# Performance work log

Hardware: AMD Instinct MI355X
Metric: run time of the kernel (lower is better)

Reference implementation:

```python
import jax, jax.numpy as jnp
import numpy as np
import math

LMAX = 3
NCHAN = 32
NEDGE = 50000

# ---------- Wigner 3j (real spherical-harmonic basis), replicating e3nn ----------

def _su2_cg(j1, j2, j3):
    f = math.factorial
    def coeff(m1, m2, m3):
        vmin = int(max(-j1 + j2 + m3, -j1 + m1, 0))
        vmax = int(min(j2 + j3 + m1, j3 - j1 + j2, j3 + m3))
        C = ((2 * j3 + 1) * f(j3 + j1 - j2) * f(j3 - j1 + j2) * f(j1 + j2 - j3) / f(j1 + j2 + j3 + 1)) ** 0.5
        C *= (f(j3 + m3) * f(j3 - m3) * f(j1 - m1) * f(j1 + m1) * f(j2 - m2) * f(j2 + m2)) ** 0.5
        S = 0.0
        for v in range(vmin, vmax + 1):
            S += (-1.0) ** (v + j2 + m2) * f(j2 + j3 + m1 - v) * f(j1 - m1 + v) / (
                f(v) * f(j3 - j1 + j2 - v) * f(j3 + m3 - v) * f(v + j1 - j2 - m3))
        return C * S
    out = np.zeros((2 * j1 + 1, 2 * j2 + 1, 2 * j3 + 1))
    for m1 in range(-j1, j1 + 1):
        for m2 in range(-j2, j2 + 1):
            m3 = m1 + m2
            if -j3 <= m3 <= j3:
                out[m1 + j1, m2 + j2, m3 + j3] = coeff(m1, m2, m3)
    return out

def _q_real_to_complex(l):
    q = np.zeros((2 * l + 1, 2 * l + 1), dtype=np.complex128)
    for m in range(-l, 0):
        q[l + m, l + abs(m)] = 1 / 2 ** 0.5
        q[l + m, l - abs(m)] = -1j / 2 ** 0.5
    q[l, l] = 1.0
    for m in range(1, l + 1):
        q[l + m, l + abs(m)] = (-1) ** m / 2 ** 0.5
        q[l + m, l - abs(m)] = 1j * (-1) ** m / 2 ** 0.5
    return (-1j) ** l * q

def _wigner_3j(l1, l2, l3):
    C = _su2_cg(l1, l2, l3).astype(np.complex128)
    Q1, Q2, Q3 = _q_real_to_complex(l1), _q_real_to_complex(l2), _q_real_to_complex(l3)
    C = np.einsum('ij,kl,mn,ikn->jlm', Q1, Q2, np.conj(Q3.T), C)
    C = np.real(C)
    return C / np.linalg.norm(C)

# ---------- Instruction enumeration (matches the torch module's __init__) ----------

def _build_paths():
    ls = list(range(LMAX + 1))  # irreps 0e,1o,2e,3o -> parity (-1)^l
    ins = []
    for l1 in ls:
        for l2 in ls:
            for l3 in range(abs(l1 - l2), min(l1 + l2, LMAX) + 1):
                if (l1 + l2 + l3) % 2 == 0:  # parity selection p1*p2 == p3
                    ins.append((l1, l2, l3))
    # e3nn Irreps.sort: stable sort of output blocks by ir; pos[i] = sorted position
    order_sorted = sorted(range(len(ins)), key=lambda i: ins[i][2])
    pos = [0] * len(ins)
    for new, old in enumerate(order_sorted):
        pos[old] = new
    # replicate `outputs.insert(ins.i_out, output)` over instruction iteration order
    concat = []
    for idx in range(len(ins)):
        concat.insert(min(pos[idx], len(concat)), idx)
    offs = np.cumsum([0] + [2 * l + 1 for l in ls]).tolist()  # block offsets in dim-16 layout
    # path_weight: component normalization, one path per output block -> sqrt(2*l3+1)
    cg = [jnp.asarray((_wigner_3j(l1, l2, l3) * math.sqrt(2 * l3 + 1)).astype(np.float32))
          for (l1, l2, l3) in ins]
    return ins, pos, concat, offs, cg

_INS, _POS, _CONCAT, _OFFS, _CG = _build_paths()  # 23 instructions, out dim 99


def setup_inputs() -> dict:
    key = jax.random.key(0)
    k1, k2, k3 = jax.random.split(key, 3)
    x = jax.random.normal(k1, (NEDGE, NCHAN, 16), dtype=jnp.float32)
    y = jax.random.normal(k2, (NEDGE, 1, 16), dtype=jnp.float32)
    weights = jax.random.normal(k3, (NEDGE, len(_INS) * NCHAN, 1), dtype=jnp.float32)
    return {"x": x, "y": y, "weights": weights}


def reference(x, y, weights):
    # x: [E, C, 16], y: [E, 1, 16], weights: [E, n_ins*C, 1]
    C = x.shape[1]
    y2 = y[:, 0, :]  # [E, 16]
    outs = [None] * len(_INS)
    for idx, (l1, l2, l3) in enumerate(_INS):
        o1, o2 = _OFFS[l1], _OFFS[l2]
        xb = x[:, :, o1:o1 + 2 * l1 + 1]            # [E, C, 2l1+1]
        yb = y2[:, o2:o2 + 2 * l2 + 1]              # [E, 2l2+1]
        w = weights[:, _POS[idx] * C:(_POS[idx] + 1) * C, 0]  # [E, C]
        # dense CG contraction == sparse gather-multiply-index_add over (mu1,mu2,mu3)
        blk = jnp.einsum('eci,ej,ijk->eck', xb, yb, _CG[idx])  # [E, C, 2l3+1]
        outs[idx] = w[:, :, None] * blk
    return jnp.concatenate([outs[i] for i in _CONCAT], axis=-1)  # [E, C, 99]
```

## Files before the change

### kernel.cpp

```cpp
#include <hip/hip_runtime.h>
#include <math.h>

#define NPATH 23
#define NEDGE 50000
#define NCHAN 32
#define NWROW 736
#define OUTW  99
#define CGTOT 1875
#define TTOT  439
#define EPB   2

constexpr int L1[NPATH]    = {0,0,0,0,1,1,1,1,1,1,2,2,2,2,2,2,2,3,3,3,3,3,3};
constexpr int L2[NPATH]    = {0,1,2,3,0,1,1,2,2,3,0,1,1,2,2,3,3,0,1,2,2,3,3};
constexpr int L3[NPATH]    = {0,1,2,3,1,0,2,1,3,2,2,1,3,0,2,1,3,3,2,1,3,0,2};
constexpr int POS[NPATH]   = {0,4,10,17,5,1,11,6,18,12,13,7,19,2,14,8,20,21,15,9,22,3,16};
constexpr int OOFF[NPATH]  = {0,4,7,12,19,1,34,22,39,46,51,31,61,2,73,25,78,85,68,28,92,3,56};
constexpr int CGOFF[NPATH] = {0,1,10,35,84,93,102,147,192,297,402,427,472,577,602,727,832,1077,1126,1231,1336,1581,1630};
constexpr int TOFF[NPATH]  = {0,1,4,9,16,25,28,43,52,73,88,113,128,163,168,193,208,243,292,327,348,397,404};
constexpr int LOFF[4]      = {0,1,4,9};

constexpr unsigned GMASK[4] = {0xE0010u, 0x700100u, 0x7C00u, 0x182EFu};

__device__ __forceinline__ int imx(int a, int b){ return a > b ? a : b; }
__device__ __forceinline__ int imn(int a, int b){ return a < b ? a : b; }

__device__ __forceinline__ double factd(int n){
    double r = 1.0;
    for(int i = 2; i <= n; ++i) r *= (double)i;
    return r;
}

__global__ __launch_bounds__(512) void cg_setup(float* __restrict__ cg_out){
    const int p  = blockIdx.x;
    const int j1 = L1[p], j2 = L2[p], j3 = L3[p];
    const int n1 = 2*j1+1, n2 = 2*j2+1, n3 = 2*j3+1;
    const int ntot = n1*n2*n3;
    const int t = threadIdx.x;

    __shared__ double scg[343];
    __shared__ double qre[3][49];
    __shared__ double qim[3][49];
    __shared__ double red[512];

    if(t < ntot){
        int a   = t / (n2*n3);
        int rem = t - a*(n2*n3);
        int b   = rem / n3;
        int g   = rem - b*n3;
        int m1 = a - j1, m2 = b - j2, m3 = g - j3;
        double val = 0.0;
        if(m1 + m2 == m3){
            int vmin = imx(imx(-j1 + j2 + m3, -j1 + m1), 0);
            int vmax = imn(imn(j2 + j3 + m1, j3 - j1 + j2), j3 + m3);
            double C = sqrt((2.0*j3 + 1.0) * factd(j3 + j1 - j2) * factd(j3 - j1 + j2)
                            * factd(j1 + j2 - j3) / factd(j1 + j2 + j3 + 1));
            C *= sqrt(factd(j3 + m3) * factd(j3 - m3) * factd(j1 - m1)
                      * factd(j1 + m1) * factd(j2 - m2) * factd(j2 + m2));
            double S = 0.0;
            for(int v = vmin; v <= vmax; ++v){
                double sgn = ((v + j2 + m2) & 1) ? -1.0 : 1.0;
                S += sgn * factd(j2 + j3 + m1 - v) * factd(j1 - m1 + v)
                     / (factd(v) * factd(j3 - j1 + j2 - v) * factd(j3 + m3 - v)
                        * factd(v + j1 - j2 - m3));
            }
            val = C * S;
        }
        scg[t] = val;
    }

    if(t < 3){
        int l = (t == 0) ? j1 : ((t == 1) ? j2 : j3);
        int n = 2*l + 1;
        double* QR = qre[t];
        double* QI = qim[t];
        for(int i = 0; i < 49; ++i){ QR[i] = 0.0; QI[i] = 0.0; }
        const double is2 = 0.70710678118654752440;
        for(int m = -l; m < 0; ++m){
            QR[(l+m)*n + (l-m)] = is2;
            QI[(l+m)*n + (l+m)] = -is2;
        }
        QR[l*n + l] = 1.0;
        for(int m = 1; m <= l; ++m){
            double s = (m & 1) ? -1.0 : 1.0;
            QR[(l+m)*n + (l+m)] = s * is2;
            QI[(l+m)*n + (l-m)] = s * is2;
        }
        double fr, fi;
        switch(l & 3){
            case 0: fr = 1.0;  fi = 0.0;  break;
            case 1: fr = 0.0;  fi = -1.0; break;
            case 2: fr = -1.0; fi = 0.0;  break;
            default: fr = 0.0; fi = 1.0;  break;
        }
        for(int i = 0; i < n*n; ++i){
            double re = QR[i], im = QI[i];
            QR[i] = re*fr - im*fi;
            QI[i] = re*fi + im*fr;
        }
    }
    __syncthreads();

    double val = 0.0;
    if(t < ntot){
        int j   = t / (n2*n3);
        int rem = t - j*(n2*n3);
        int lq  = rem / n3;
        int m   = rem - lq*n3;
        double acc = 0.0;
        for(int i = 0; i < n1; ++i){
            double q1r = qre[0][i*n1 + j], q1i = qim[0][i*n1 + j];
            if(q1r == 0.0 && q1i == 0.0) continue;
            for(int k = 0; k < n2; ++k){
                double q2r = qre[1][k*n2 + lq], q2i = qim[1][k*n2 + lq];
                if(q2r == 0.0 && q2i == 0.0) continue;
                double ar = q1r*q2r - q1i*q2i;
                double ai = q1r*q2i + q1i*q2r;
                for(int n = 0; n < n3; ++n){
                    double cv = scg[(i*n2 + k)*n3 + n];
                    if(cv == 0.0) continue;
                    double q3r = qre[2][n*n3 + m];
                    double q3i = -qim[2][n*n3 + m];
                    acc += cv * (ar*q3r - ai*q3i);
                }
            }
        }
        val = acc;
    }

    red[t] = val * val;
    __syncthreads();
    for(int s = 256; s > 0; s >>= 1){
        if(t < s) red[t] += red[t + s];
        __syncthreads();
    }
    double nrm = sqrt(red[0]);
    if(t < ntot){
        cg_out[CGOFF[p] + t] = (float)(val * sqrt(2.0*j3 + 1.0) / nrm);
    }
}

template<int G>
__device__ __forceinline__ void phaseC(const float* __restrict__ xr,
                                       const float* __restrict__ wreg,
                                       const float* __restrict__ Te,
                                       float* __restrict__ ob)
{
    constexpr unsigned mask = GMASK[G];
    #pragma unroll
    for(int p = 0; p < NPATH; ++p){
        if(!((mask >> p) & 1u)) continue;
        const int n1 = 2*L1[p] + 1;
        const int n3 = 2*L3[p] + 1;
        const int o1 = LOFF[L1[p]];
        const float wp = wreg[p];
        const float* Tp = Te + TOFF[p];
        #pragma unroll
        for(int k = 0; k < n3; ++k){
            float acc = 0.f;
            #pragma unroll
            for(int i = 0; i < n1; ++i)
                acc = fmaf(xr[o1 + i], Tp[i*n3 + k], acc);
            ob[OOFF[p] + k] = wp * acc;
        }
    }
}

__global__ __launch_bounds__(256, 5) void tp_main(
    const float* __restrict__ x, const float* __restrict__ y,
    const float* __restrict__ w, const float* __restrict__ cg,
    float* __restrict__ out)
{
    __shared__ __align__(16) float obuf[EPB*NCHAN*OUTW];
    __shared__ float Ts[EPB*TTOT];
    __shared__ float ys[EPB*16];

    const int tid = threadIdx.x;
    const int e0  = blockIdx.x * EPB;

    const int c   = tid & 31;
    const int el  = (tid >> 5) & 1;
    const int grp = tid >> 6;
    const int e   = e0 + el;

    const float4* xp = reinterpret_cast<const float4*>(x + (size_t)(e*NCHAN + c)*16);
    float4 x0 = xp[0], x1 = xp[1], x2 = xp[2], x3 = xp[3];

    const float* wrow = w + (size_t)e*NWROW + c;
    float wreg[NPATH];
    #pragma unroll
    for(int p = 0; p < NPATH; ++p)
        wreg[p] = wrow[POS[p]*NCHAN];

    if(tid < EPB*16) ys[tid] = y[e0*16 + tid];
    __syncthreads();

    for(int u = tid; u < EPB*TTOT; u += 256){
        int eli = u / TTOT;
        int v   = u - eli*TTOT;
        int p   = 0;
        while(p < NPATH-1 && TOFF[p+1] <= v) ++p;
        int rel = v - TOFF[p];
        int n2  = 2*L2[p] + 1;
        int n3  = 2*L3[p] + 1;
        int i   = rel / n3;
        int k   = rel - i*n3;
        int o2  = LOFF[L2[p]];
        const float* cgp = &cg[CGOFF[p]];
        float acc = 0.f;
        for(int j = 0; j < n2; ++j)
            acc += ys[eli*16 + o2 + j] * cgp[(i*n2 + j)*n3 + k];
        Ts[u] = acc;
    }
    __syncthreads();

    float xr[16];
    xr[0]=x0.x;  xr[1]=x0.y;  xr[2]=x0.z;  xr[3]=x0.w;
    xr[4]=x1.x;  xr[5]=x1.y;  xr[6]=x1.z;  xr[7]=x1.w;
    xr[8]=x2.x;  xr[9]=x2.y;  xr[10]=x2.z; xr[11]=x2.w;
    xr[12]=x3.x; xr[13]=x3.y; xr[14]=x3.z; xr[15]=x3.w;

    const float* Te = Ts + el*TTOT;
    float* ob = obuf + el*(NCHAN*OUTW) + c*OUTW;

    switch(grp){
        case 0: phaseC<0>(xr, wreg, Te, ob); break;
        case 1: phaseC<1>(xr, wreg, Te, ob); break;
        case 2: phaseC<2>(xr, wreg, Te, ob); break;
        default: phaseC<3>(xr, wreg, Te, ob); break;
    }
    __syncthreads();

    const float4* ob4 = reinterpret_cast<const float4*>(obuf);
    float4* o4 = reinterpret_cast<float4*>(out + (size_t)blockIdx.x * (EPB*NCHAN*OUTW));
    #pragma unroll
    for(int idx = tid; idx < EPB*NCHAN*OUTW/4; idx += 256)
        o4[idx] = ob4[idx];
}

extern "C" void kernel_launch(void* const* d_in, const int* in_sizes, int n_in,
                              void* d_out, int out_size, void* d_ws, size_t ws_size,
                              hipStream_t stream)
{
    const float* x  = (const float*)d_in[0];
    const float* y  = (const float*)d_in[1];
    const float* wt = (const float*)d_in[2];
    float* out = (float*)d_out;
    float* cgw = (float*)d_ws;

    cg_setup<<<NPATH, 512, 0, stream>>>(cgw);
    tp_main<<<NEDGE/EPB, 256, 0, stream>>>(x, y, wt, cgw, out);
}
```

Baseline: 285.1 us.

## Stage output tile in fp16, densify CG table, trim per-group weight loads

The shared-memory output staging buffer becomes _Float16 and is widened back to fp32 when written to global memory, halving LDS footprint so more blocks fit per CU (launch bounds raised to 8 blocks). The CG setup now emits a dense 16-wide padded row per (path,i,k) slot, so the per-edge T computation becomes a fixed unrolled 16-term dot with no path search. Each thread group also loads only the weights for its own paths (at most 10) through a precomputed offset table instead of all 23. Rounding outputs through fp16 loses precision and may exceed tolerance.

```diff
diff --git a/kernel.cpp b/kernel.cpp
--- a/kernel.cpp
+++ b/kernel.cpp
@@ -6,20 +6,27 @@
 #define NCHAN 32
 #define NWROW 736
 #define OUTW  99
-#define CGTOT 1875
 #define TTOT  439
 #define EPB   2
+#define NTHR  256
 
 constexpr int L1[NPATH]    = {0,0,0,0,1,1,1,1,1,1,2,2,2,2,2,2,2,3,3,3,3,3,3};
 constexpr int L2[NPATH]    = {0,1,2,3,0,1,1,2,2,3,0,1,1,2,2,3,3,0,1,2,2,3,3};
 constexpr int L3[NPATH]    = {0,1,2,3,1,0,2,1,3,2,2,1,3,0,2,1,3,3,2,1,3,0,2};
 constexpr int POS[NPATH]   = {0,4,10,17,5,1,11,6,18,12,13,7,19,2,14,8,20,21,15,9,22,3,16};
 constexpr int OOFF[NPATH]  = {0,4,7,12,19,1,34,22,39,46,51,31,61,2,73,25,78,85,68,28,92,3,56};
-constexpr int CGOFF[NPATH] = {0,1,10,35,84,93,102,147,192,297,402,427,472,577,602,727,832,1077,1126,1231,1336,1581,1630};
 constexpr int TOFF[NPATH]  = {0,1,4,9,16,25,28,43,52,73,88,113,128,163,168,193,208,243,292,327,348,397,404};
 constexpr int LOFF[4]      = {0,1,4,9};
 
-constexpr unsigned GMASK[4] = {0xE0010u, 0x700100u, 0x7C00u, 0x182EFu};
+constexpr unsigned GMASK4[4] = {0xE0010u, 0x700100u, 0x7C00u, 0x182EFu};
+constexpr int GWOFF[4][10] = {
+    {160, 672, 480, 288,   0,   0,   0,   0,   0,   0},
+    {576, 704,  96, 512,   0,   0,   0,   0,   0,   0},
+    {416, 224, 608,  64, 448,   0,   0,   0,   0,   0},
+    {  0, 128, 320, 544,  32, 352, 192, 384, 256, 640},
+};
+
+typedef _Float16 __attribute__((ext_vector_type(4))) h4;
 
 __device__ __forceinline__ int imx(int a, int b){ return a > b ? a : b; }
 __device__ __forceinline__ int imn(int a, int b){ return a < b ? a : b; }
@@ -30,10 +37,11 @@
     return r;
 }
 
-__global__ __launch_bounds__(512) void cg_setup(float* __restrict__ cg_out){
+__global__ __launch_bounds__(512) void cg_setup(float* __restrict__ cgd2){
     const int p  = blockIdx.x;
     const int j1 = L1[p], j2 = L2[p], j3 = L3[p];
     const int n1 = 2*j1+1, n2 = 2*j2+1, n3 = 2*j3+1;
+    const int o2 = LOFF[j2];
     const int ntot = n1*n2*n3;
     const int t = threadIdx.x;
 
@@ -129,13 +137,19 @@
 
     red[t] = val * val;
     __syncthreads();
-    for(int s = 256; s > 0; s >>= 1){
-        if(t < s) red[t] += red[t + s];
+    if(t < 343) scg[t] = val;
+    for(int s2 = 256; s2 > 0; s2 >>= 1){
+        if(t < s2) red[t] += red[t + s2];
         __syncthreads();
     }
-    double nrm = sqrt(red[0]);
-    if(t < ntot){
-        cg_out[CGOFF[p] + t] = (float)(val * sqrt(2.0*j3 + 1.0) / nrm);
+    const double scale = sqrt(2.0*j3 + 1.0) / sqrt(red[0]);
+
+    for(int u = t; u < n1*n3*16; u += 512){
+        int sl = u >> 4, jf = u & 15;
+        int i  = sl / n3, k = sl - i*n3;
+        int j  = jf - o2;
+        double v2 = (j >= 0 && j < n2) ? scg[(i*n2 + j)*n3 + k] : 0.0;
+        cgd2[(size_t)(TOFF[p] + sl)*16 + jf] = (float)(v2 * scale);
     }
 }
 
@@ -143,16 +157,17 @@
 __device__ __forceinline__ void phaseC(const float* __restrict__ xr,
                                        const float* __restrict__ wreg,
                                        const float* __restrict__ Te,
-                                       float* __restrict__ ob)
+                                       _Float16* __restrict__ ob)
 {
-    constexpr unsigned mask = GMASK[G];
+    constexpr unsigned mask = GMASK4[G];
     #pragma unroll
     for(int p = 0; p < NPATH; ++p){
         if(!((mask >> p) & 1u)) continue;
+        const int widx = __builtin_popcount(mask & ((1u << p) - 1u));
         const int n1 = 2*L1[p] + 1;
         const int n3 = 2*L3[p] + 1;
         const int o1 = LOFF[L1[p]];
-        const float wp = wreg[p];
+        const float wp = wreg[widx];
         const float* Tp = Te + TOFF[p];
         #pragma unroll
         for(int k = 0; k < n3; ++k){
@@ -160,17 +175,17 @@
             #pragma unroll
             for(int i = 0; i < n1; ++i)
                 acc = fmaf(xr[o1 + i], Tp[i*n3 + k], acc);
-            ob[OOFF[p] + k] = wp * acc;
-        }
-    }
-}
-
-__global__ __launch_bounds__(256, 5) void tp_main(
+            ob[OOFF[p] + k] = (_Float16)(wp * acc);
+        }
+    }
+}
+
+__global__ __launch_bounds__(NTHR, 8) void tp_main(
     const float* __restrict__ x, const float* __restrict__ y,
-    const float* __restrict__ w, const float* __restrict__ cg,
+    const float* __restrict__ w, const float* __restrict__ cgd2,
     float* __restrict__ out)
 {
-    __shared__ __align__(16) float obuf[EPB*NCHAN*OUTW];
+    __shared__ __align__(16) _Float16 obuf[EPB*NCHAN*OUTW];
     __shared__ float Ts[EPB*TTOT];
     __shared__ float ys[EPB*16];
 
@@ -185,30 +200,23 @@
     const float4* xp = reinterpret_cast<const float4*>(x + (size_t)(e*NCHAN + c)*16);
     float4 x0 = xp[0], x1 = xp[1], x2 = xp[2], x3 = xp[3];
 
-    const float* wrow = w + (size_t)e*NWROW + c;
-    float wreg[NPATH];
+    const float* wbase = w + (size_t)e*NWROW + c;
+    float wreg[10];
     #pragma unroll
-    for(int p = 0; p < NPATH; ++p)
-        wreg[p] = wrow[POS[p]*NCHAN];
+    for(int k = 0; k < 10; ++k)
+        wreg[k] = wbase[GWOFF[grp][k]];
 
     if(tid < EPB*16) ys[tid] = y[e0*16 + tid];
     __syncthreads();
 
-    for(int u = tid; u < EPB*TTOT; u += 256){
+    for(int u = tid; u < EPB*TTOT; u += NTHR){
         int eli = u / TTOT;
-        int v   = u - eli*TTOT;
-        int p   = 0;
-        while(p < NPATH-1 && TOFF[p+1] <= v) ++p;
-        int rel = v - TOFF[p];
-        int n2  = 2*L2[p] + 1;
-        int n3  = 2*L3[p] + 1;
-        int i   = rel / n3;
-        int k   = rel - i*n3;
-        int o2  = LOFF[L2[p]];
-        const float* cgp = &cg[CGOFF[p]];
+        int s   = u - eli*TTOT;
+        const float* cr = cgd2 + (size_t)s*16;
         float acc = 0.f;
-        for(int j = 0; j < n2; ++j)
-            acc += ys[eli*16 + o2 + j] * cgp[(i*n2 + j)*n3 + k];
+        #pragma unroll
+        for(int j = 0; j < 16; ++j)
+            acc = fmaf(ys[eli*16 + j], cr[j], acc);
         Ts[u] = acc;
     }
     __syncthreads();
@@ -220,7 +228,7 @@
     xr[12]=x3.x; xr[13]=x3.y; xr[14]=x3.z; xr[15]=x3.w;
 
     const float* Te = Ts + el*TTOT;
-    float* ob = obuf + el*(NCHAN*OUTW) + c*OUTW;
+    _Float16* ob = obuf + el*(NCHAN*OUTW) + c*OUTW;
 
     switch(grp){
         case 0: phaseC<0>(xr, wreg, Te, ob); break;
@@ -230,11 +238,17 @@
     }
     __syncthreads();
 
-    const float4* ob4 = reinterpret_cast<const float4*>(obuf);
+    const h4* ob4 = reinterpret_cast<const h4*>(obuf);
     float4* o4 = reinterpret_cast<float4*>(out + (size_t)blockIdx.x * (EPB*NCHAN*OUTW));
     #pragma unroll
-    for(int idx = tid; idx < EPB*NCHAN*OUTW/4; idx += 256)
-        o4[idx] = ob4[idx];
+    for(int k2 = 0; k2 < 7; ++k2){
+        int idx = tid + k2*NTHR;
+        if(idx < EPB*NCHAN*OUTW/4){
+            h4 hv = ob4[idx];
+            float4 fv = { (float)hv[0], (float)hv[1], (float)hv[2], (float)hv[3] };
+            o4[idx] = fv;
+        }
+    }
 }
 
 extern "C" void kernel_launch(void* const* d_in, const int* in_sizes, int n_in,
@@ -245,8 +259,8 @@
     const float* y  = (const float*)d_in[1];
     const float* wt = (const float*)d_in[2];
     float* out = (float*)d_out;
-    float* cgw = (float*)d_ws;
-
-    cg_setup<<<NPATH, 512, 0, stream>>>(cgw);
-    tp_main<<<NEDGE/EPB, 256, 0, stream>>>(x, y, wt, cgw, out);
-}
+    float* cgd2 = (float*)d_ws;
+
+    cg_setup<<<NPATH, 512, 0, stream>>>(cgd2);
+    tp_main<<<NEDGE/EPB, NTHR, 0, stream>>>(x, y, wt, cgd2, out);
+}
```

Result: slower. 310.3 us (+8.8%).
